# Kernel tuning notes

Hardware: AMD Instinct MI355X
Metric: run time of the kernel (lower is better)

## Reference

```python
import jax, jax.numpy as jnp
import numpy as np

VOCAB, EMB, LAT, MAXLEN, BATCH = 2048, 256, 64, 32, 64
SIZE_LAT = 3.0  # size_lat_dim: initial upper bound of every latent dimension


def setup_inputs() -> dict:
    key = jax.random.key(0)
    k0, k1, k2, k3 = jax.random.split(key, 4)
    tokens = jax.random.randint(k0, (BATCH, MAXLEN), 1, VOCAB, dtype=jnp.int32)  # avoid PAD=0
    emb = jax.random.normal(k1, (VOCAB, EMB), jnp.float32) * 0.02
    Wx = jax.random.normal(k2, (EMB, 4 * VOCAB), jnp.float32) * (1.0 / np.sqrt(EMB))
    Wh = jax.random.normal(k3, (VOCAB, 4 * VOCAB), jnp.float32) * (1.0 / np.sqrt(VOCAB))
    b = jnp.zeros((4 * VOCAB,), jnp.float32)
    return {"tokens": tokens, "emb": emb, "Wx": Wx, "Wh": Wh, "b": b}


def _lstm_step(x, h, c, Wx, Wh, b):
    # Keras LSTM gate order: i, f, g(candidate), o
    z = x @ Wx + h @ Wh + b
    i, f, g, o = jnp.split(z, 4, axis=-1)
    c = jax.nn.sigmoid(f) * c + jax.nn.sigmoid(i) * jnp.tanh(g)
    h = jax.nn.sigmoid(o) * jnp.tanh(c)
    return h, c


def reference(tokens, emb, Wx, Wh, b):
    B = tokens.shape[0]
    low0 = jnp.zeros((B, LAT), jnp.float32)
    upp0 = jnp.full((B, LAT), SIZE_LAT, jnp.float32)
    h0 = jnp.zeros((B, VOCAB), jnp.float32)  # empty (all-PAD) prefix -> zero LSTM output -> uniform softmax
    c0 = jnp.zeros((B, VOCAB), jnp.float32)
    dims = jnp.arange(LAT)

    def step(carry, tok):
        low, upp, h, c, d = carry
        # LM distribution over next token given prefix consumed so far
        probs = jax.nn.softmax(h, axis=-1)                      # [B, V]
        cum = jnp.cumsum(probs, axis=-1)
        c_upp = jnp.take_along_axis(cum, tok[:, None], axis=-1)[:, 0]
        c_low = c_upp - jnp.take_along_axis(probs, tok[:, None], axis=-1)[:, 0]
        # arithmetic-coding bound update on current latent dimension d only
        mask = dims == d                                         # [LAT]
        rng = jnp.sum(jnp.where(mask, upp - low, 0.0), axis=-1)  # [B] range at dim d
        base = jnp.sum(jnp.where(mask, low, 0.0), axis=-1)       # [B] low at dim d
        low = jnp.where(mask[None, :], (base + rng * c_low)[:, None], low)
        upp = jnp.where(mask[None, :], (base + rng * c_upp)[:, None], upp)
        z = 0.5 * (low + upp)                                    # mean of stacked bounds
        # advance embedded LM by one token (equivalent to re-running it on the prefix)
        h, c = _lstm_step(emb[tok], h, c, Wx, Wh, b)
        d = (d + 1) % LAT
        return (low, upp, h, c, d), z

    _, zs = jax.lax.scan(step, (low0, upp0, h0, c0, jnp.int32(0)), tokens.T)
    return jnp.transpose(zs, (1, 0, 2))  # [B, MAXLEN, LAT]
```

## Files before the change

kernel.cpp:

```cpp
#include <hip/hip_runtime.h>
#include <hip/hip_bf16.h>

#define VOCAB 2048
#define EMBD  256
#define LATD  64
#define TLEN  32
#define BATCH 64
#define NBLK  256
#define NCG   128

typedef __attribute__((ext_vector_type(8))) short bf16x8;
typedef __attribute__((ext_vector_type(4))) float f32x4;

__global__ void k_init(ushort* __restrict__ h0, unsigned* __restrict__ arrv) {
  int i = blockIdx.x * 256 + threadIdx.x;
  h0[i] = 0;
  if (i < 384) arrv[i] = 0;
}

__global__ void k_transpose(const float* __restrict__ src,
                            __hip_bfloat16* __restrict__ dst, int K) {
  __shared__ __hip_bfloat16 tile[64][72];
  int k0 = (blockIdx.x >> 7) * 64;
  int n0 = (blockIdx.x & 127) * 64;
  int tid = threadIdx.x;
  {
    int kl = tid >> 2;
    int nq = (tid & 3) << 4;
    const float* s = src + (size_t)(k0 + kl) * 8192 + n0 + nq;
#pragma unroll
    for (int i = 0; i < 4; ++i) {
      float4 v = *reinterpret_cast<const float4*>(s + i * 4);
      tile[nq + i * 4 + 0][kl] = __float2bfloat16(v.x);
      tile[nq + i * 4 + 1][kl] = __float2bfloat16(v.y);
      tile[nq + i * 4 + 2][kl] = __float2bfloat16(v.z);
      tile[nq + i * 4 + 3][kl] = __float2bfloat16(v.w);
    }
  }
  __syncthreads();
  {
    int nl = tid >> 2;
    int kq = (tid & 3) << 4;
    uint4* d = reinterpret_cast<uint4*>(dst + (size_t)(n0 + nl) * K + k0 + kq);
    const uint4* s = reinterpret_cast<const uint4*>(&tile[nl][kq]);
    d[0] = s[0];
    d[1] = s[1];
  }
}

__global__ void k_gather(const int* __restrict__ tokens,
                         const float* __restrict__ emb,
                         __hip_bfloat16* __restrict__ xb) {
  int tid = threadIdx.x;
  int row = blockIdx.x * 4 + (tid >> 6);
  int lane = tid & 63;
  int t = row >> 6, b = row & 63;
  int tok = tokens[b * TLEN + t];
  float4 v = *reinterpret_cast<const float4*>(emb + (size_t)tok * EMBD + lane * 4);
  __hip_bfloat16* d = xb + (size_t)row * EMBD + lane * 4;
  d[0] = __float2bfloat16(v.x);
  d[1] = __float2bfloat16(v.y);
  d[2] = __float2bfloat16(v.z);
  d[3] = __float2bfloat16(v.w);
}

__device__ __forceinline__ void store_agent_u32(unsigned* p, unsigned v) {
  __hip_atomic_store(p, v, __ATOMIC_RELAXED, __HIP_MEMORY_SCOPE_AGENT);
}
__device__ __forceinline__ unsigned load_agent_u32(const unsigned* p) {
  return __hip_atomic_load(p, __ATOMIC_RELAXED, __HIP_MEMORY_SCOPE_AGENT);
}
__device__ __forceinline__ unsigned long long load_agent_u64(const void* p) {
  return __hip_atomic_load((const unsigned long long*)p, __ATOMIC_RELAXED,
                           __HIP_MEMORY_SCOPE_AGENT);
}
__device__ __forceinline__ void store_agent_f32(float* p, float v) {
  __hip_atomic_store(p, v, __ATOMIC_RELAXED, __HIP_MEMORY_SCOPE_AGENT);
}
__device__ __forceinline__ float2 load_agent_f32x2(const float* p) {
  unsigned long long u = load_agent_u64(p);
  float2 f;
  __builtin_memcpy(&f, &u, 8);
  return f;
}
__device__ __forceinline__ unsigned short bf16_bits(float x) {
  __hip_bfloat16 h = __float2bfloat16(x);
  unsigned short u;
  __builtin_memcpy(&u, &h, 2);
  return u;
}

__device__ __forceinline__ void grid_barrier(unsigned* arrv, unsigned* rel,
                                             int t, int j, int tid, int lane,
                                             int wid) {
  __syncthreads();
  const unsigned want = (unsigned)(t + 1);
  if (j == 0) {
    if (wid == 0) {
      if (lane == 0) store_agent_u32(arrv, want);
      for (;;) {
        unsigned long long a = load_agent_u64(arrv + 2 * lane);
        unsigned long long b = load_agent_u64(arrv + 128 + 2 * lane);
        bool ok = ((unsigned)a >= want) && ((unsigned)(a >> 32) >= want) &&
                  ((unsigned)b >= want) && ((unsigned)(b >> 32) >= want);
        if (__all(ok)) break;
      }
      if (lane < 8) store_agent_u32(rel + (lane << 4), want);
    }
  } else {
    if (tid == 0) {
      store_agent_u32(arrv + j, want);
      while (load_agent_u32(rel + ((j & 7) << 4)) < want)
        __builtin_amdgcn_s_sleep(1);
    }
  }
  __syncthreads();
}

__global__ __launch_bounds__(512, 1) void k_persist(
    const int* __restrict__ tokens,
    const __hip_bfloat16* __restrict__ WhT,
    const __hip_bfloat16* __restrict__ WxT,
    const __hip_bfloat16* __restrict__ xb,
    const float* __restrict__ bias,
    __hip_bfloat16* __restrict__ hring,
    float* __restrict__ stats,
    float* __restrict__ out,
    unsigned* __restrict__ arrv,
    unsigned* __restrict__ rel) {
  const int tid = threadIdx.x;
  const int lane = tid & 63;
  const int wid = tid >> 6;
  const int j = blockIdx.x;
  const int cg = j >> 1;
  const int rg = j & 1;
  const int r0 = rg << 5;

  __shared__ float racc[8][2][4][4][64];
  __shared__ float sval[TLEN];

  const int rr = lane & 15;
  const int kg = lane >> 4;

  bf16x8 Bf[9][4];
#pragma unroll
  for (int it = 0; it < 8; ++it) {
    int kb = (wid * 8 + it) * 32 + kg * 8;
#pragma unroll
    for (int gt = 0; gt < 4; ++gt)
      Bf[it][gt] = *(const bf16x8*)(WhT + (size_t)((gt << 11) + (cg << 4) + rr) * VOCAB + kb);
  }
  {
    int kx = wid * 32 + kg * 8;
#pragma unroll
    for (int gt = 0; gt < 4; ++gt)
      Bf[8][gt] = *(const bf16x8*)(WxT + (size_t)((gt << 11) + (cg << 4) + rr) * EMBD + kx);
  }

  const int m_e = wid >> 2;
  const int r_e = wid & 3;
  const int rowg = r0 + m_e * 16 + kg * 4 + r_e;
  const int v = (cg << 4) + rr;
  float bias_r[4];
#pragma unroll
  for (int gt = 0; gt < 4; ++gt) bias_r[gt] = bias[gt * 2048 + v];
  float c_reg = 0.f;

  for (int t = 0; t < TLEN; ++t) {
    const int par = t & 1;
    const __hip_bfloat16* hcur = hring + (size_t)t * (BATCH * VOCAB);
    __hip_bfloat16* hnext = (__hip_bfloat16*)hring + (size_t)(t + 1) * (BATCH * VOCAB);
    const int tnext = (t + 1 < TLEN) ? t + 1 : TLEN - 1;
    const int tok = tokens[rowg * TLEN + tnext];

    if (j < BATCH && wid == 0) {
      float val;
      if (t == 0) {
        int tk = tokens[j * TLEN];
        val = 1.5f * (2.f * tk + 1.f) * (1.f / 2048.f);
      } else {
        const float* st = stats + par * 3 * BATCH * NCG;
        float2 u0 = load_agent_f32x2(st + (0 * BATCH + j) * NCG + lane * 2);
        float2 u1 = load_agent_f32x2(st + (1 * BATCH + j) * NCG + lane * 2);
        float2 u2 = load_agent_f32x2(st + (2 * BATCH + j) * NCG + lane * 2);
        float a0 = u0.x + u0.y, a1 = u1.x + u1.y, a2 = u2.x + u2.y;
#pragma unroll
        for (int mm = 1; mm <= 32; mm <<= 1) {
          a0 += __shfl_xor(a0, mm);
          a1 += __shfl_xor(a1, mm);
          a2 += __shfl_xor(a2, mm);
        }
        val = 1.5f * (2.f * a1 + a2) / a0;
      }
      if (lane == t) sval[t] = val;
    }

    f32x4 acc[2][4];
#pragma unroll
    for (int mf = 0; mf < 2; ++mf)
#pragma unroll
      for (int gt = 0; gt < 4; ++gt) acc[mf][gt] = (f32x4){0.f, 0.f, 0.f, 0.f};

    bf16x8 Ar[2][2];
    auto issue = [&](int it) {
      int slot = it & 1;
      if (it < 8) {
        int kb = (wid * 8 + it) * 32 + kg * 8;
        const __hip_bfloat16* p = hcur + kb;
        Ar[slot][0] = *(const bf16x8*)(p + (r0 + rr) * VOCAB);
        Ar[slot][1] = *(const bf16x8*)(p + (r0 + 16 + rr) * VOCAB);
      } else {
        int kx = wid * 32 + kg * 8;
        const __hip_bfloat16* p = xb + (size_t)t * BATCH * EMBD + kx;
        Ar[slot][0] = *(const bf16x8*)(p + (r0 + rr) * EMBD);
        Ar[slot][1] = *(const bf16x8*)(p + (r0 + 16 + rr) * EMBD);
      }
    };

    issue(0);
#pragma unroll
    for (int it = 0; it < 9; ++it) {
      if (it + 1 < 9) issue(it + 1);
      const int sl = it & 1;
#pragma unroll
      for (int gt = 0; gt < 4; ++gt) {
        acc[0][gt] = __builtin_amdgcn_mfma_f32_16x16x32_bf16(Ar[sl][0], Bf[it][gt], acc[0][gt], 0, 0, 0);
        acc[1][gt] = __builtin_amdgcn_mfma_f32_16x16x32_bf16(Ar[sl][1], Bf[it][gt], acc[1][gt], 0, 0, 0);
      }
    }

#pragma unroll
    for (int mf = 0; mf < 2; ++mf)
#pragma unroll
      for (int gt = 0; gt < 4; ++gt)
#pragma unroll
        for (int r = 0; r < 4; ++r) racc[wid][mf][gt][r][lane] = acc[mf][gt][r];
    __syncthreads();

    float z[4];
#pragma unroll
    for (int gt = 0; gt < 4; ++gt) {
      float s = bias_r[gt];
#pragma unroll
      for (int w = 0; w < 8; ++w) s += racc[w][m_e][gt][r_e][lane];
      z[gt] = s;
    }
    float gi = 1.f / (1.f + __expf(-z[0]));
    float gf = 1.f / (1.f + __expf(-z[1]));
    float go = 1.f / (1.f + __expf(-z[3]));
    float cnew = gf * c_reg + gi * tanhf(z[2]);
    float hn = go * tanhf(cnew);
    c_reg = cnew;

    {
      unsigned b0 = bf16_bits(hn);
      unsigned q0 = (unsigned)__shfl_xor((int)b0, 1);
      if (!(rr & 1))
        store_agent_u32((unsigned*)(hnext + rowg * VOCAB + v), b0 | (q0 << 16));
    }

    float e = __expf(hn);
    float sl = (v < tok) ? e : 0.f;
    float st = (v == tok) ? e : 0.f;
#pragma unroll
    for (int mm = 1; mm <= 8; mm <<= 1) {
      e += __shfl_xor(e, mm);
      sl += __shfl_xor(sl, mm);
      st += __shfl_xor(st, mm);
    }
    if (rr == 0) {
      float* stn = stats + (par ^ 1) * 3 * BATCH * NCG;
      store_agent_f32(&stn[(0 * BATCH + rowg) * NCG + cg], e);
      store_agent_f32(&stn[(1 * BATCH + rowg) * NCG + cg], sl);
      store_agent_f32(&stn[(2 * BATCH + rowg) * NCG + cg], st);
    }

    if (t < TLEN - 1) grid_barrier(arrv, rel, t, j, tid, lane, wid);
  }

  if (j < BATCH) {
    __syncthreads();
    for (int idx = tid; idx < TLEN * LATD; idx += 512) {
      int tp = idx >> 6, d = idx & 63;
      out[j * TLEN * LATD + idx] = (d < TLEN && d <= tp) ? sval[d] : 1.5f;
    }
  }
}

extern "C" void kernel_launch(void* const* d_in, const int* in_sizes, int n_in,
                              void* d_out, int out_size, void* d_ws, size_t ws_size,
                              hipStream_t stream) {
  (void)in_sizes; (void)n_in; (void)out_size; (void)ws_size;
  const int* tokens = (const int*)d_in[0];
  const float* emb  = (const float*)d_in[1];
  const float* Wx   = (const float*)d_in[2];
  const float* Wh   = (const float*)d_in[3];
  const float* bias = (const float*)d_in[4];
  float* out = (float*)d_out;
  char* ws = (char*)d_ws;

  __hip_bfloat16* WhT = (__hip_bfloat16*)(ws);
  __hip_bfloat16* WxT = (__hip_bfloat16*)(ws + 33554432);
  __hip_bfloat16* xb  = (__hip_bfloat16*)(ws + 37748736);
  __hip_bfloat16* hr  = (__hip_bfloat16*)(ws + 38797312);
  float* stats        = (float*)(ws + 47448064);
  unsigned* arrv      = (unsigned*)(ws + 47644672);
  unsigned* rel       = (unsigned*)(ws + 47645696);

  k_init<<<512, 256, 0, stream>>>((ushort*)hr, arrv);
  k_transpose<<<4096, 256, 0, stream>>>(Wh, WhT, 2048);
  k_transpose<<<512, 256, 0, stream>>>(Wx, WxT, 256);
  k_gather<<<512, 256, 0, stream>>>(tokens, emb, xb);
  k_persist<<<NBLK, 512, 0, stream>>>(tokens, WhT, WxT, xb, bias, hr, stats, out, arrv, rel);
}
```

Measured before the change: 255.3 us.

## Use all-to-all polling grid barrier and deepen A-operand prefetch pipeline

Replaces the two-level grid barrier, where block 0 gathers arrivals and publishes release flags, with a flat barrier in which every block's first wave polls all arrival counters directly. This removes one release hop per step at the cost of more polling traffic on the counters. The A-operand loads now run three slots deep instead of double-buffered, with base pointers hoisted out of the loop. Weight preload uses opaque inline-asm loads followed by one explicit waitcnt, to keep the compiler from rescheduling or spilling them.

```diff
diff --git a/kernel.cpp b/kernel.cpp
--- a/kernel.cpp
+++ b/kernel.cpp
@@ -15,7 +15,7 @@
 __global__ void k_init(ushort* __restrict__ h0, unsigned* __restrict__ arrv) {
   int i = blockIdx.x * 256 + threadIdx.x;
   h0[i] = 0;
-  if (i < 384) arrv[i] = 0;
+  if (i < NBLK) arrv[i] = 0;
 }
 
 __global__ void k_transpose(const float* __restrict__ src,
@@ -67,9 +67,6 @@
 __device__ __forceinline__ void store_agent_u32(unsigned* p, unsigned v) {
   __hip_atomic_store(p, v, __ATOMIC_RELAXED, __HIP_MEMORY_SCOPE_AGENT);
 }
-__device__ __forceinline__ unsigned load_agent_u32(const unsigned* p) {
-  return __hip_atomic_load(p, __ATOMIC_RELAXED, __HIP_MEMORY_SCOPE_AGENT);
-}
 __device__ __forceinline__ unsigned long long load_agent_u64(const void* p) {
   return __hip_atomic_load((const unsigned long long*)p, __ATOMIC_RELAXED,
                            __HIP_MEMORY_SCOPE_AGENT);
@@ -89,29 +86,25 @@
   __builtin_memcpy(&u, &h, 2);
   return u;
 }
-
-__device__ __forceinline__ void grid_barrier(unsigned* arrv, unsigned* rel,
-                                             int t, int j, int tid, int lane,
-                                             int wid) {
+__device__ __forceinline__ bf16x8 load_opaque(const __hip_bfloat16* p) {
+  bf16x8 r;
+  asm volatile("global_load_dwordx4 %0, %1, off" : "=&v"(r) : "v"(p));
+  return r;
+}
+
+__device__ __forceinline__ void grid_barrier(unsigned* arrv, int t, int j,
+                                             int tid, int lane) {
   __syncthreads();
   const unsigned want = (unsigned)(t + 1);
-  if (j == 0) {
-    if (wid == 0) {
-      if (lane == 0) store_agent_u32(arrv, want);
-      for (;;) {
-        unsigned long long a = load_agent_u64(arrv + 2 * lane);
-        unsigned long long b = load_agent_u64(arrv + 128 + 2 * lane);
-        bool ok = ((unsigned)a >= want) && ((unsigned)(a >> 32) >= want) &&
-                  ((unsigned)b >= want) && ((unsigned)(b >> 32) >= want);
-        if (__all(ok)) break;
-      }
-      if (lane < 8) store_agent_u32(rel + (lane << 4), want);
-    }
-  } else {
-    if (tid == 0) {
-      store_agent_u32(arrv + j, want);
-      while (load_agent_u32(rel + ((j & 7) << 4)) < want)
-        __builtin_amdgcn_s_sleep(1);
+  if (tid < 64) {
+    if (lane == 0) store_agent_u32(arrv + j, want);
+    for (;;) {
+      unsigned long long a = load_agent_u64(arrv + 2 * lane);
+      unsigned long long b = load_agent_u64(arrv + 128 + 2 * lane);
+      bool ok = ((unsigned)a >= want) && ((unsigned)(a >> 32) >= want) &&
+                ((unsigned)b >= want) && ((unsigned)(b >> 32) >= want);
+      if (__all(ok)) break;
+      __builtin_amdgcn_s_sleep(2);
     }
   }
   __syncthreads();
@@ -126,8 +119,7 @@
     __hip_bfloat16* __restrict__ hring,
     float* __restrict__ stats,
     float* __restrict__ out,
-    unsigned* __restrict__ arrv,
-    unsigned* __restrict__ rel) {
+    unsigned* __restrict__ arrv) {
   const int tid = threadIdx.x;
   const int lane = tid & 63;
   const int wid = tid >> 6;
@@ -148,14 +140,16 @@
     int kb = (wid * 8 + it) * 32 + kg * 8;
 #pragma unroll
     for (int gt = 0; gt < 4; ++gt)
-      Bf[it][gt] = *(const bf16x8*)(WhT + (size_t)((gt << 11) + (cg << 4) + rr) * VOCAB + kb);
+      Bf[it][gt] = load_opaque(WhT + (size_t)((gt << 11) + (cg << 4) + rr) * VOCAB + kb);
   }
   {
     int kx = wid * 32 + kg * 8;
 #pragma unroll
     for (int gt = 0; gt < 4; ++gt)
-      Bf[8][gt] = *(const bf16x8*)(WxT + (size_t)((gt << 11) + (cg << 4) + rr) * EMBD + kx);
-  }
+      Bf[8][gt] = load_opaque(WxT + (size_t)((gt << 11) + (cg << 4) + rr) * EMBD + kx);
+  }
+  asm volatile("s_waitcnt vmcnt(0)" ::: "memory");
+  __builtin_amdgcn_sched_barrier(0);
 
   const int m_e = wid >> 2;
   const int r_e = wid & 3;
@@ -201,32 +195,32 @@
 #pragma unroll
       for (int gt = 0; gt < 4; ++gt) acc[mf][gt] = (f32x4){0.f, 0.f, 0.f, 0.f};
 
-    bf16x8 Ar[2][2];
+    const __hip_bfloat16* aBase = hcur + (size_t)(r0 + rr) * VOCAB + wid * 256 + kg * 8;
+    const __hip_bfloat16* xBase = xb + (size_t)t * BATCH * EMBD +
+                                  (size_t)(r0 + rr) * EMBD + wid * 32 + kg * 8;
+    bf16x8 Ar[3][2];
     auto issue = [&](int it) {
-      int slot = it & 1;
+      int slot = it % 3;
       if (it < 8) {
-        int kb = (wid * 8 + it) * 32 + kg * 8;
-        const __hip_bfloat16* p = hcur + kb;
-        Ar[slot][0] = *(const bf16x8*)(p + (r0 + rr) * VOCAB);
-        Ar[slot][1] = *(const bf16x8*)(p + (r0 + 16 + rr) * VOCAB);
+        Ar[slot][0] = *(const bf16x8*)(aBase + it * 32);
+        Ar[slot][1] = *(const bf16x8*)(aBase + 16 * VOCAB + it * 32);
       } else {
-        int kx = wid * 32 + kg * 8;
-        const __hip_bfloat16* p = xb + (size_t)t * BATCH * EMBD + kx;
-        Ar[slot][0] = *(const bf16x8*)(p + (r0 + rr) * EMBD);
-        Ar[slot][1] = *(const bf16x8*)(p + (r0 + 16 + rr) * EMBD);
+        Ar[slot][0] = *(const bf16x8*)(xBase);
+        Ar[slot][1] = *(const bf16x8*)(xBase + 16 * EMBD);
       }
     };
 
-    issue(0);
+#pragma unroll
+    for (int it = 0; it < 3; ++it) issue(it);
 #pragma unroll
     for (int it = 0; it < 9; ++it) {
-      if (it + 1 < 9) issue(it + 1);
-      const int sl = it & 1;
+      const int sl = it % 3;
 #pragma unroll
       for (int gt = 0; gt < 4; ++gt) {
         acc[0][gt] = __builtin_amdgcn_mfma_f32_16x16x32_bf16(Ar[sl][0], Bf[it][gt], acc[0][gt], 0, 0, 0);
         acc[1][gt] = __builtin_amdgcn_mfma_f32_16x16x32_bf16(Ar[sl][1], Bf[it][gt], acc[1][gt], 0, 0, 0);
       }
+      if (it + 3 < 9) issue(it + 3);
     }
 
 #pragma unroll
@@ -275,7 +269,7 @@
       store_agent_f32(&stn[(2 * BATCH + rowg) * NCG + cg], st);
     }
 
-    if (t < TLEN - 1) grid_barrier(arrv, rel, t, j, tid, lane, wid);
+    if (t < TLEN - 1) grid_barrier(arrv, t, j, tid, lane);
   }
 
   if (j < BATCH) {
@@ -305,11 +299,10 @@
   __hip_bfloat16* hr  = (__hip_bfloat16*)(ws + 38797312);
   float* stats        = (float*)(ws + 47448064);
   unsigned* arrv      = (unsigned*)(ws + 47644672);
-  unsigned* rel       = (unsigned*)(ws + 47645696);
 
   k_init<<<512, 256, 0, stream>>>((ushort*)hr, arrv);
   k_transpose<<<4096, 256, 0, stream>>>(Wh, WhT, 2048);
   k_transpose<<<512, 256, 0, stream>>>(Wx, WxT, 256);
   k_gather<<<512, 256, 0, stream>>>(tokens, emb, xb);
-  k_persist<<<NBLK, 512, 0, stream>>>(tokens, WhT, WxT, xb, bias, hr, stats, out, arrv, rel);
-}
+  k_persist<<<NBLK, 512, 0, stream>>>(tokens, WhT, WxT, xb, bias, hr, stats, out, arrv);
+}
```

Result: slower. 353.4 us (+38.4%).

## Stream Wh weights per step with 4-deep prefetch instead of register-resident tiles

Applied to the files above, without the earlier changes.

Drops the 36 register-resident bf16x8 weight fragments per thread and reloads the Wh/Wx tiles from memory every timestep through a 4-deep register prefetch ring, alongside the h activations. Block-to-column-group mapping is permuted so neighbouring blocks share row groups differently, likely for L2/XCD locality. Stats reduction is split across three waves, and the final value computation is deferred to the end of the kernel. This cuts register pressure but adds per-step weight traffic of about 16 MB bf16 per step, which must come from L2/MALL.

```diff
diff --git a/kernel.cpp b/kernel.cpp
--- a/kernel.cpp
+++ b/kernel.cpp
@@ -91,12 +91,11 @@
 }
 
 __device__ __forceinline__ void grid_barrier(unsigned* arrv, unsigned* rel,
-                                             int t, int j, int tid, int lane,
-                                             int wid) {
+                                             int t, int j, int tid, int lane) {
   __syncthreads();
   const unsigned want = (unsigned)(t + 1);
   if (j == 0) {
-    if (wid == 0) {
+    if (tid < 64) {
       if (lane == 0) store_agent_u32(arrv, want);
       for (;;) {
         unsigned long long a = load_agent_u64(arrv + 2 * lane);
@@ -132,30 +131,25 @@
   const int lane = tid & 63;
   const int wid = tid >> 6;
   const int j = blockIdx.x;
-  const int cg = j >> 1;
-  const int rg = j & 1;
+  const int cg = (j & 7) | ((j >> 4) << 3);
+  const int rg = (j >> 3) & 1;
   const int r0 = rg << 5;
 
   __shared__ float racc[8][2][4][4][64];
+  __shared__ float spart[TLEN][3];
   __shared__ float sval[TLEN];
 
   const int rr = lane & 15;
   const int kg = lane >> 4;
 
-  bf16x8 Bf[9][4];
-#pragma unroll
-  for (int it = 0; it < 8; ++it) {
-    int kb = (wid * 8 + it) * 32 + kg * 8;
-#pragma unroll
-    for (int gt = 0; gt < 4; ++gt)
-      Bf[it][gt] = *(const bf16x8*)(WhT + (size_t)((gt << 11) + (cg << 4) + rr) * VOCAB + kb);
-  }
-  {
-    int kx = wid * 32 + kg * 8;
-#pragma unroll
-    for (int gt = 0; gt < 4; ++gt)
-      Bf[8][gt] = *(const bf16x8*)(WxT + (size_t)((gt << 11) + (cg << 4) + rr) * EMBD + kx);
-  }
+  const __hip_bfloat16* bBase[4];
+#pragma unroll
+  for (int gt = 0; gt < 4; ++gt)
+    bBase[gt] = WhT + (size_t)((gt << 11) + (cg << 4) + rr) * VOCAB + wid * 256 + kg * 8;
+  const __hip_bfloat16* bxBase[4];
+#pragma unroll
+  for (int gt = 0; gt < 4; ++gt)
+    bxBase[gt] = WxT + (size_t)((gt << 11) + (cg << 4) + rr) * EMBD + wid * 32 + kg * 8;
 
   const int m_e = wid >> 2;
   const int r_e = wid & 3;
@@ -173,60 +167,51 @@
     const int tnext = (t + 1 < TLEN) ? t + 1 : TLEN - 1;
     const int tok = tokens[rowg * TLEN + tnext];
 
-    if (j < BATCH && wid == 0) {
-      float val;
-      if (t == 0) {
-        int tk = tokens[j * TLEN];
-        val = 1.5f * (2.f * tk + 1.f) * (1.f / 2048.f);
+    float2 sv;
+    const bool do_stat = (t > 0) && (j < BATCH) && (wid < 3);
+    if (do_stat)
+      sv = load_agent_f32x2(stats + par * 3 * BATCH * NCG +
+                            (wid * BATCH + j) * NCG + lane * 2);
+
+    f32x4 acc[2][4];
+#pragma unroll
+    for (int mf = 0; mf < 2; ++mf)
+#pragma unroll
+      for (int gt = 0; gt < 4; ++gt) acc[mf][gt] = (f32x4){0.f, 0.f, 0.f, 0.f};
+
+    const __hip_bfloat16* aBase = hcur + (size_t)(r0 + rr) * VOCAB + wid * 256 + kg * 8;
+    const __hip_bfloat16* xBase = xb + (size_t)t * BATCH * EMBD +
+                                  (size_t)(r0 + rr) * EMBD + wid * 32 + kg * 8;
+    bf16x8 Ar[4][2];
+    bf16x8 Br[4][4];
+    auto issue = [&](int it) {
+      int slot = it & 3;
+      if (it < 8) {
+        Ar[slot][0] = *(const bf16x8*)(aBase + it * 32);
+        Ar[slot][1] = *(const bf16x8*)(aBase + 16 * VOCAB + it * 32);
+#pragma unroll
+        for (int gt = 0; gt < 4; ++gt)
+          Br[slot][gt] = *(const bf16x8*)(bBase[gt] + it * 32);
       } else {
-        const float* st = stats + par * 3 * BATCH * NCG;
-        float2 u0 = load_agent_f32x2(st + (0 * BATCH + j) * NCG + lane * 2);
-        float2 u1 = load_agent_f32x2(st + (1 * BATCH + j) * NCG + lane * 2);
-        float2 u2 = load_agent_f32x2(st + (2 * BATCH + j) * NCG + lane * 2);
-        float a0 = u0.x + u0.y, a1 = u1.x + u1.y, a2 = u2.x + u2.y;
-#pragma unroll
-        for (int mm = 1; mm <= 32; mm <<= 1) {
-          a0 += __shfl_xor(a0, mm);
-          a1 += __shfl_xor(a1, mm);
-          a2 += __shfl_xor(a2, mm);
-        }
-        val = 1.5f * (2.f * a1 + a2) / a0;
-      }
-      if (lane == t) sval[t] = val;
-    }
-
-    f32x4 acc[2][4];
-#pragma unroll
-    for (int mf = 0; mf < 2; ++mf)
-#pragma unroll
-      for (int gt = 0; gt < 4; ++gt) acc[mf][gt] = (f32x4){0.f, 0.f, 0.f, 0.f};
-
-    bf16x8 Ar[2][2];
-    auto issue = [&](int it) {
-      int slot = it & 1;
-      if (it < 8) {
-        int kb = (wid * 8 + it) * 32 + kg * 8;
-        const __hip_bfloat16* p = hcur + kb;
-        Ar[slot][0] = *(const bf16x8*)(p + (r0 + rr) * VOCAB);
-        Ar[slot][1] = *(const bf16x8*)(p + (r0 + 16 + rr) * VOCAB);
-      } else {
-        int kx = wid * 32 + kg * 8;
-        const __hip_bfloat16* p = xb + (size_t)t * BATCH * EMBD + kx;
-        Ar[slot][0] = *(const bf16x8*)(p + (r0 + rr) * EMBD);
-        Ar[slot][1] = *(const bf16x8*)(p + (r0 + 16 + rr) * EMBD);
+        Ar[slot][0] = *(const bf16x8*)(xBase);
+        Ar[slot][1] = *(const bf16x8*)(xBase + 16 * EMBD);
+#pragma unroll
+        for (int gt = 0; gt < 4; ++gt)
+          Br[slot][gt] = *(const bf16x8*)(bxBase[gt]);
       }
     };
 
-    issue(0);
+#pragma unroll
+    for (int it = 0; it < 4; ++it) issue(it);
 #pragma unroll
     for (int it = 0; it < 9; ++it) {
-      if (it + 1 < 9) issue(it + 1);
-      const int sl = it & 1;
+      const int sl = it & 3;
 #pragma unroll
       for (int gt = 0; gt < 4; ++gt) {
-        acc[0][gt] = __builtin_amdgcn_mfma_f32_16x16x32_bf16(Ar[sl][0], Bf[it][gt], acc[0][gt], 0, 0, 0);
-        acc[1][gt] = __builtin_amdgcn_mfma_f32_16x16x32_bf16(Ar[sl][1], Bf[it][gt], acc[1][gt], 0, 0, 0);
+        acc[0][gt] = __builtin_amdgcn_mfma_f32_16x16x32_bf16(Ar[sl][0], Br[sl][gt], acc[0][gt], 0, 0, 0);
+        acc[1][gt] = __builtin_amdgcn_mfma_f32_16x16x32_bf16(Ar[sl][1], Br[sl][gt], acc[1][gt], 0, 0, 0);
       }
+      if (it + 4 < 9) issue(it + 4);
     }
 
 #pragma unroll
@@ -236,6 +221,13 @@
 #pragma unroll
         for (int r = 0; r < 4; ++r) racc[wid][mf][gt][r][lane] = acc[mf][gt][r];
     __syncthreads();
+
+    if (do_stat) {
+      float a = sv.x + sv.y;
+#pragma unroll
+      for (int mm = 1; mm <= 32; mm <<= 1) a += __shfl_xor(a, mm);
+      if (lane == 0) spart[t][wid] = a;
+    }
 
     float z[4];
 #pragma unroll
@@ -275,10 +267,24 @@
       store_agent_f32(&stn[(2 * BATCH + rowg) * NCG + cg], st);
     }
 
-    if (t < TLEN - 1) grid_barrier(arrv, rel, t, j, tid, lane, wid);
+    if (t < TLEN - 1) grid_barrier(arrv, rel, t, j, tid, lane);
   }
 
   if (j < BATCH) {
+    __syncthreads();
+    if (tid < TLEN) {
+      float val;
+      if (tid == 0) {
+        int tk = tokens[j * TLEN];
+        val = 1.5f * (2.f * tk + 1.f) * (1.f / 2048.f);
+      } else {
+        float S  = spart[tid][0];
+        float SL = spart[tid][1];
+        float ST = spart[tid][2];
+        val = 1.5f * (2.f * SL + ST) / S;
+      }
+      sval[tid] = val;
+    }
     __syncthreads();
     for (int idx = tid; idx < TLEN * LATD; idx += 512) {
       int tp = idx >> 6, d = idx & 63;
```

Result: slower. 270.2 us (+5.9%).
